# Performance work log

Measured on AMD Instinct MI355X. Metric: run time of the kernel, lower is better.

The kernel has to match this reference:

```python
import jax, jax.numpy as jnp
import numpy as np

ALPHA = 0.1
K = 10
N_NODES = 100000
N_EDGES = 3200000


def setup_inputs() -> dict:
    key = jax.random.key(0)
    ks = jax.random.split(key, 8)
    feat = jax.random.normal(ks[0], (N_NODES, 512), dtype=jnp.float32)
    W1 = jax.random.normal(ks[1], (512, 256), dtype=jnp.float32) * (1.0 / np.sqrt(512))
    b1 = jnp.zeros((256,), dtype=jnp.float32)
    W2 = jax.random.normal(ks[2], (256, 64), dtype=jnp.float32) * (1.0 / np.sqrt(256))
    b2 = jnp.zeros((64,), dtype=jnp.float32)
    edge_vals = jax.random.uniform(ks[3], (N_EDGES,), dtype=jnp.float32) / 32.0  # ~row-normalized
    edge_row = jax.random.randint(ks[4], (N_EDGES,), 0, N_NODES, dtype=jnp.int32)
    edge_col = jax.random.randint(ks[5], (N_EDGES,), 0, N_NODES, dtype=jnp.int32)
    return {"features": feat, "W1": W1, "b1": b1, "W2": W2, "b2": b2,
            "edge_vals": edge_vals, "edge_row": edge_row, "edge_col": edge_col}


def _spmm(edge_vals, edge_row, edge_col, x):
    # out[r] = sum_e vals[e] * x[col[e]]  for edges with row[e]==r
    msgs = edge_vals[:, None] * x[edge_col]  # [E, C]
    return jax.ops.segment_sum(msgs, edge_row, num_segments=N_NODES)


def reference(features, W1, b1, W2, b2, edge_vals, edge_row, edge_col):
    # MLP (dropout is identity in eval mode)
    x = jax.nn.relu(features @ W1 + b1)        # [N, nhid]
    x = x @ W2 + b2                             # [N, num_classes]
    h = x
    for _ in range(K):
        x = (1.0 - ALPHA) * _spmm(edge_vals, edge_row, edge_col, x) + ALPHA * h
    return jax.nn.log_softmax(x, axis=1)
```

## Files before the change

### kernel.cpp

```cpp
#include <hip/hip_runtime.h>
#include <hip/hip_bf16.h>
#include <math.h>

#define NNODES 100000
#define NFEAT 512
#define NHID 256
#define NCLS 64
#define ALPHA_C 0.1f
#define NBUCKET 512
#define NPB 512
#define RB2 196

typedef short s16x8 __attribute__((ext_vector_type(8)));
typedef float f32x4 __attribute__((ext_vector_type(4)));

__device__ inline unsigned short f2b(float f) {
    union { float f; unsigned u; } v; v.f = f;
    unsigned r = v.u + 0x7fff + ((v.u >> 16) & 1);
    return (unsigned short)(r >> 16);
}
__device__ inline float b2f(unsigned short b) {
    return __uint_as_float((unsigned)b << 16);
}
__device__ inline float blo(unsigned u) { return __uint_as_float(u << 16); }
__device__ inline float bhi(unsigned u) { return __uint_as_float(u & 0xffff0000u); }

__global__ __launch_bounds__(256) void cvtT_kernel(
    const float* __restrict__ src, unsigned short* __restrict__ dst, int R, int Clog2)
{
    int idx = blockIdx.x * 256 + threadIdx.x;
    int C = 1 << Clog2;
    if (idx < R * C) {
        int r = idx >> Clog2, c = idx & (C - 1);
        dst[(size_t)c * R + r] = f2b(src[idx]);
    }
}

#define HID_STRIDE 264

__global__ __launch_bounds__(256) void mlp_mfma_kernel(
    const float* __restrict__ feat, const unsigned short* __restrict__ W1T,
    const float* __restrict__ b1, const unsigned short* __restrict__ W2T,
    const float* __restrict__ b2, unsigned short* __restrict__ h, int N)
{
    __shared__ unsigned short hid_s[64 * HID_STRIDE];
    const int tid  = threadIdx.x;
    const int w    = tid >> 6;
    const int lane = tid & 63;
    const int lr   = lane & 15;
    const int lh   = lane >> 4;
    const int m0   = blockIdx.x * 64;

    f32x4 acc[4][4];
#pragma unroll
    for (int i = 0; i < 4; ++i)
#pragma unroll
        for (int j = 0; j < 4; ++j) acc[i][j] = (f32x4)0.f;

    const float* arow[4];
#pragma unroll
    for (int mi = 0; mi < 4; ++mi) {
        int r = m0 + mi * 16 + lr;
        if (r > N - 1) r = N - 1;
        arow[mi] = feat + (size_t)r * NFEAT;
    }
    const unsigned short* brow[4];
#pragma unroll
    for (int nj = 0; nj < 4; ++nj)
        brow[nj] = W1T + (size_t)(w * 64 + nj * 16 + lr) * NFEAT;

    for (int kb = 0; kb < NFEAT; kb += 32) {
        const int k0 = kb + lh * 8;
        s16x8 afr[4], bfr[4];
#pragma unroll
        for (int mi = 0; mi < 4; ++mi) {
            float4 f0 = *reinterpret_cast<const float4*>(arow[mi] + k0);
            float4 f1 = *reinterpret_cast<const float4*>(arow[mi] + k0 + 4);
            s16x8 a;
            a[0] = f2b(f0.x); a[1] = f2b(f0.y); a[2] = f2b(f0.z); a[3] = f2b(f0.w);
            a[4] = f2b(f1.x); a[5] = f2b(f1.y); a[6] = f2b(f1.z); a[7] = f2b(f1.w);
            afr[mi] = a;
        }
#pragma unroll
        for (int nj = 0; nj < 4; ++nj)
            bfr[nj] = *reinterpret_cast<const s16x8*>(brow[nj] + k0);
#pragma unroll
        for (int mi = 0; mi < 4; ++mi)
#pragma unroll
            for (int nj = 0; nj < 4; ++nj)
                acc[mi][nj] = __builtin_amdgcn_mfma_f32_16x16x32_bf16(
                    afr[mi], bfr[nj], acc[mi][nj], 0, 0, 0);
    }

#pragma unroll
    for (int nj = 0; nj < 4; ++nj) {
        int col = w * 64 + nj * 16 + lr;
        float bias = b1[col];
#pragma unroll
        for (int mi = 0; mi < 4; ++mi)
#pragma unroll
            for (int q = 0; q < 4; ++q) {
                int row = mi * 16 + lh * 4 + q;
                hid_s[row * HID_STRIDE + col] = f2b(fmaxf(acc[mi][nj][q] + bias, 0.f));
            }
    }
    __syncthreads();

    f32x4 acc2[4];
#pragma unroll
    for (int i = 0; i < 4; ++i) acc2[i] = (f32x4)0.f;
    const int cw = w * 16;
    const unsigned short* b2row = W2T + (size_t)(cw + lr) * NHID;
    for (int ks = 0; ks < NHID; ks += 32) {
        int k0 = ks + lh * 8;
        s16x8 bfr = *reinterpret_cast<const s16x8*>(b2row + k0);
#pragma unroll
        for (int mi = 0; mi < 4; ++mi) {
            s16x8 afr = *reinterpret_cast<const s16x8*>(
                &hid_s[(mi * 16 + lr) * HID_STRIDE + k0]);
            acc2[mi] = __builtin_amdgcn_mfma_f32_16x16x32_bf16(afr, bfr, acc2[mi], 0, 0, 0);
        }
    }
    int col = cw + lr;
    float bias2 = b2[col];
#pragma unroll
    for (int mi = 0; mi < 4; ++mi)
#pragma unroll
        for (int q = 0; q < 4; ++q) {
            int row = m0 + mi * 16 + lh * 4 + q;
            if (row < N) h[(size_t)row * NCLS + col] = f2b(acc2[mi][q] + bias2);
        }
}

__global__ __launch_bounds__(1024) void scanA_kernel(
    const int* __restrict__ cnt, int* __restrict__ excl, int* __restrict__ partials, int n)
{
    __shared__ int wsum[16];
    const int t = threadIdx.x, wid = t >> 6, lane = t & 63;
    const int i = blockIdx.x * 1024 + t;
    int c = (i < n) ? cnt[i] : 0;
    int x = c;
#pragma unroll
    for (int off = 1; off < 64; off <<= 1) {
        int y = __shfl_up(x, off);
        if (lane >= off) x += y;
    }
    if (lane == 63) wsum[wid] = x;
    __syncthreads();
    if (wid == 0 && lane < 16) {
        int wv = wsum[lane];
#pragma unroll
        for (int off = 1; off < 16; off <<= 1) {
            int y = __shfl_up(wv, off);
            if (lane >= off) wv += y;
        }
        wsum[lane] = wv;
    }
    __syncthreads();
    int woff = wid ? wsum[wid - 1] : 0;
    int incl = x + woff;
    if (i < n) excl[i] = incl - c;
    if (t == 1023) partials[blockIdx.x] = incl;
}

__global__ __launch_bounds__(256) void scanB_kernel(
    int* __restrict__ partials, int* __restrict__ total_out, int nb, int n)
{
    __shared__ int s[256];
    const int t = threadIdx.x;
    int v = (t < nb) ? partials[t] : 0;
    s[t] = v;
    __syncthreads();
    for (int off = 1; off < 256; off <<= 1) {
        int y = (t >= off) ? s[t - off] : 0;
        __syncthreads();
        s[t] += y;
        __syncthreads();
    }
    partials[t] = s[t] - v;
    if (t == 255) total_out[n] = s[255];
}

__global__ __launch_bounds__(1024) void scanC_kernel(
    int* __restrict__ arr, const int* __restrict__ partials, int n)
{
    const int i = blockIdx.x * 1024 + threadIdx.x;
    if (i < n) arr[i] += partials[blockIdx.x];
}

__global__ __launch_bounds__(256) void countP1_kernel(
    const int* __restrict__ erow, int* __restrict__ cnts, int E, int CE)
{
    __shared__ int c[NBUCKET];
    const int blk = blockIdx.x, t = threadIdx.x;
    for (int i = t; i < NBUCKET; i += 256) c[i] = 0;
    __syncthreads();
    const int e0 = blk * CE, e1 = min(e0 + CE, E);
    for (int e = e0 + t; e < e1; e += 256)
        atomicAdd(&c[erow[e] / RB2], 1);
    __syncthreads();
    for (int b = t; b < NBUCKET; b += 256)
        cnts[(size_t)b * NPB + blk] = c[b];
}

__global__ __launch_bounds__(256) void scatterA_kernel(
    const float* __restrict__ vals, const int* __restrict__ erow,
    const int* __restrict__ ecol, const int* __restrict__ S,
    unsigned long long* __restrict__ stage, int E, int CE)
{
    __shared__ int lcur[NBUCKET];
    const int blk = blockIdx.x, t = threadIdx.x;
    for (int b = t; b < NBUCKET; b += 256) lcur[b] = S[(size_t)b * NPB + blk];
    __syncthreads();
    const int e0 = blk * CE, e1 = min(e0 + CE, E);
    for (int e = e0 + t; e < e1; e += 256) {
        int r = erow[e];
        unsigned q = (unsigned)__float2int_rn(vals[e] * 1048576.f);
        if (q > 32767u) q = 32767u;
        unsigned lo = ((unsigned)ecol[e] << 15) | q;
        int pos = atomicAdd(&lcur[r / RB2], 1);
        stage[pos] = ((unsigned long long)(unsigned)r << 32) | lo;
    }
}

__global__ __launch_bounds__(256) void scatterB_kernel(
    const unsigned long long* __restrict__ stage, const int* __restrict__ S,
    unsigned* __restrict__ ep, int* __restrict__ row_ptr, int n, int E)
{
    __shared__ int hcnt[256];
    __shared__ int lcur[256];
    const int b = blockIdx.x, t = threadIdx.x;
    if (b == 0 && t == 0) row_ptr[n] = E;
    const int r0 = b * RB2;
    if (r0 >= n) return;
    const int nr = min(RB2, n - r0);
    const int s0 = S[(size_t)b * NPB];
    const int s1 = S[(size_t)(b + 1) * NPB];
    hcnt[t] = 0;
    __syncthreads();
    for (int i = s0 + t; i < s1; i += 256)
        atomicAdd(&hcnt[(int)(stage[i] >> 32) - r0], 1);
    __syncthreads();
    int v = hcnt[t];
    lcur[t] = v;
    __syncthreads();
    for (int off = 1; off < 256; off <<= 1) {
        int y = (t >= off) ? lcur[t - off] : 0;
        __syncthreads();
        lcur[t] += y;
        __syncthreads();
    }
    int excl = lcur[t] - v;
    if (t < nr) row_ptr[r0 + t] = s0 + excl;
    __syncthreads();
    lcur[t] = s0 + excl;
    __syncthreads();
    for (int i = s0 + t; i < s1; i += 256) {
        unsigned long long rec = stage[i];
        int p = atomicAdd(&lcur[(int)(rec >> 32) - r0], 1);
        ep[p] = (unsigned)rec;
    }
}

__global__ __launch_bounds__(256) void spmm_kernel(
    const unsigned short* __restrict__ x_in, const unsigned short* __restrict__ h,
    unsigned short* __restrict__ x_out, const int* __restrict__ row_ptr,
    const unsigned* __restrict__ ep, int n)
{
    const int wid = threadIdx.x >> 6, lane = threadIdx.x & 63;
    const int r = blockIdx.x * 4 + wid;
    if (r >= n) return;
    const int g  = lane >> 4;
    const int li = lane & 15;
    const int s = row_ptr[r], e_end = row_ptr[r + 1];

    float aA0 = 0.f, aA1 = 0.f, aA2 = 0.f, aA3 = 0.f;
    float aB0 = 0.f, aB1 = 0.f, aB2 = 0.f, aB3 = 0.f;
    float aC0 = 0.f, aC1 = 0.f, aC2 = 0.f, aC3 = 0.f;
    float aD0 = 0.f, aD1 = 0.f, aD2 = 0.f, aD3 = 0.f;
    int e0 = s;
    for (; e0 + 16 <= e_end; e0 += 16) {
        unsigned p1 = __builtin_nontemporal_load(ep + e0 + g);
        unsigned p2 = __builtin_nontemporal_load(ep + e0 + 4 + g);
        unsigned p3 = __builtin_nontemporal_load(ep + e0 + 8 + g);
        unsigned p4 = __builtin_nontemporal_load(ep + e0 + 12 + g);
        int   c1 = (int)(p1 >> 15);
        int   c2 = (int)(p2 >> 15);
        int   c3 = (int)(p3 >> 15);
        int   c4 = (int)(p4 >> 15);
        float v1 = (float)(p1 & 0x7fffu) * (1.f / 1048576.f);
        float v2 = (float)(p2 & 0x7fffu) * (1.f / 1048576.f);
        float v3 = (float)(p3 & 0x7fffu) * (1.f / 1048576.f);
        float v4 = (float)(p4 & 0x7fffu) * (1.f / 1048576.f);
        uint2 u1 = *reinterpret_cast<const uint2*>(x_in + ((size_t)c1 << 6) + (li << 2));
        uint2 u2 = *reinterpret_cast<const uint2*>(x_in + ((size_t)c2 << 6) + (li << 2));
        uint2 u3 = *reinterpret_cast<const uint2*>(x_in + ((size_t)c3 << 6) + (li << 2));
        uint2 u4 = *reinterpret_cast<const uint2*>(x_in + ((size_t)c4 << 6) + (li << 2));
        aA0 += v1 * blo(u1.x); aA1 += v1 * bhi(u1.x);
        aA2 += v1 * blo(u1.y); aA3 += v1 * bhi(u1.y);
        aB0 += v2 * blo(u2.x); aB1 += v2 * bhi(u2.x);
        aB2 += v2 * blo(u2.y); aB3 += v2 * bhi(u2.y);
        aC0 += v3 * blo(u3.x); aC1 += v3 * bhi(u3.x);
        aC2 += v3 * blo(u3.y); aC3 += v3 * bhi(u3.y);
        aD0 += v4 * blo(u4.x); aD1 += v4 * bhi(u4.x);
        aD2 += v4 * blo(u4.y); aD3 += v4 * bhi(u4.y);
    }
    for (; e0 < e_end; e0 += 4) {
        int e = e0 + g;
        if (e < e_end) {
            unsigned p = __builtin_nontemporal_load(ep + e);
            int   c = (int)(p >> 15);
            float v = (float)(p & 0x7fffu) * (1.f / 1048576.f);
            uint2 u = *reinterpret_cast<const uint2*>(x_in + ((size_t)c << 6) + (li << 2));
            aA0 += v * blo(u.x); aA1 += v * bhi(u.x);
            aA2 += v * blo(u.y); aA3 += v * bhi(u.y);
        }
    }
    float a0 = (aA0 + aB0) + (aC0 + aD0);
    float a1 = (aA1 + aB1) + (aC1 + aD1);
    float a2 = (aA2 + aB2) + (aC2 + aD2);
    float a3 = (aA3 + aB3) + (aC3 + aD3);
#pragma unroll
    for (int off = 16; off < 64; off <<= 1) {
        a0 += __shfl_xor(a0, off);
        a1 += __shfl_xor(a1, off);
        a2 += __shfl_xor(a2, off);
        a3 += __shfl_xor(a3, off);
    }
    if (g == 0) {
        size_t o = ((size_t)r << 6) + (li << 2);
        const unsigned* hp = reinterpret_cast<const unsigned*>(h + o);
        unsigned hx = __builtin_nontemporal_load(hp);
        unsigned hy = __builtin_nontemporal_load(hp + 1);
        float r0 = (1.f - ALPHA_C) * a0 + ALPHA_C * blo(hx);
        float r1 = (1.f - ALPHA_C) * a1 + ALPHA_C * bhi(hx);
        float r2 = (1.f - ALPHA_C) * a2 + ALPHA_C * blo(hy);
        float r3 = (1.f - ALPHA_C) * a3 + ALPHA_C * bhi(hy);
        uint2 ou;
        ou.x = ((unsigned)f2b(r1) << 16) | f2b(r0);
        ou.y = ((unsigned)f2b(r3) << 16) | f2b(r2);
        *reinterpret_cast<uint2*>(x_out + o) = ou;
    }
}

__global__ __launch_bounds__(256) void lsm_kernel(
    const unsigned short* __restrict__ x, float* __restrict__ out, int n)
{
    const int wid = threadIdx.x >> 6, lane = threadIdx.x & 63;
    const int r = blockIdx.x * 4 + wid;
    if (r >= n) return;
    float v = b2f(x[(size_t)r * NCLS + lane]);
    float m = v;
#pragma unroll
    for (int o = 32; o > 0; o >>= 1) m = fmaxf(m, __shfl_xor(m, o));
    float ex = expf(v - m);
    float s = ex;
#pragma unroll
    for (int o = 32; o > 0; o >>= 1) s += __shfl_xor(s, o);
    out[(size_t)r * NCLS + lane] = (v - m) - logf(s);
}

extern "C" void kernel_launch(void* const* d_in, const int* in_sizes, int n_in,
                              void* d_out, int out_size, void* d_ws, size_t ws_size,
                              hipStream_t stream)
{
    const float* feat = (const float*)d_in[0];
    const float* W1   = (const float*)d_in[1];
    const float* b1   = (const float*)d_in[2];
    const float* W2   = (const float*)d_in[3];
    const float* b2   = (const float*)d_in[4];
    const float* vals = (const float*)d_in[5];
    const int*   erow = (const int*)d_in[6];
    const int*   ecol = (const int*)d_in[7];
    const int N = in_sizes[0] / NFEAT;
    const int E = in_sizes[5];
    float* out = (float*)d_out;
    const int CE = (E + NPB - 1) / NPB;
    const int NC = NBUCKET * NPB;

    size_t off = 0;
    auto alloc = [&](size_t bytes) -> void* {
        void* p = (char*)d_ws + off;
        off += (bytes + 255) & ~(size_t)255;
        return p;
    };
    unsigned short*     h        = (unsigned short*)alloc((size_t)N * NCLS * 2);
    unsigned short*     xA       = (unsigned short*)alloc((size_t)N * NCLS * 2);
    unsigned short*     xB       = (unsigned short*)alloc((size_t)N * NCLS * 2);
    int*                row_ptr  = (int*)alloc((size_t)(N + 1) * 4);
    int*                cnts     = (int*)alloc((size_t)NC * 4);
    int*                S        = (int*)alloc((size_t)(NC + 1) * 4);
    int*                partials = (int*)alloc(256 * 4);
    unsigned*           ep       = (unsigned*)alloc((size_t)E * 4);
    unsigned long long* stage    = (unsigned long long*)alloc((size_t)E * 8);
    unsigned short*     W1T      = (unsigned short*)alloc((size_t)NHID * NFEAT * 2);
    unsigned short*     W2T      = (unsigned short*)alloc((size_t)NCLS * NHID * 2);
    (void)ws_size;

    cvtT_kernel<<<(NFEAT * NHID + 255) / 256, 256, 0, stream>>>(W1, W1T, NFEAT, 8);
    cvtT_kernel<<<(NHID * NCLS + 255) / 256, 256, 0, stream>>>(W2, W2T, NHID, 6);

    mlp_mfma_kernel<<<(N + 63) / 64, 256, 0, stream>>>(feat, W1T, b1, W2T, b2, h, N);

    countP1_kernel<<<NPB, 256, 0, stream>>>(erow, cnts, E, CE);
    scanA_kernel<<<NC / 1024, 1024, 0, stream>>>(cnts, S, partials, NC);
    scanB_kernel<<<1, 256, 0, stream>>>(partials, S, 256, NC);
    scanC_kernel<<<NC / 1024, 1024, 0, stream>>>(S, partials, NC);
    scatterA_kernel<<<NPB, 256, 0, stream>>>(vals, erow, ecol, S, stage, E, CE);
    scatterB_kernel<<<NBUCKET, 256, 0, stream>>>(stage, S, ep, row_ptr, N, E);

    const int gprop = (N + 3) / 4;
    const unsigned short* cur = h;
    for (int i = 0; i < 10; ++i) {
        unsigned short* dst = (i & 1) ? xB : xA;
        spmm_kernel<<<gprop, 256, 0, stream>>>(cur, h, dst, row_ptr, ep, N);
        cur = dst;
    }

    lsm_kernel<<<(N + 3) / 4, 256, 0, stream>>>(cur, out, N);
}
```

Baseline: 1.076 ms.

## Split propagation into four 16-column groups for cache-resident gathers

Stores the MLP output in a column-grouped layout of four slabs of 16 bf16 columns per node. Each slab is propagated through all ten SpMM iterations independently, so the gathered working set (about 3.2 MB per slab) can stay in L2 or the last-level cache instead of streaming 12.8 MB of random rows. The cost is four times as many launches and four times the edge-list reads, and each gather now moves only 4 bytes per lane. The log-softmax kernel is updated to read the grouped layout.

```diff
diff --git a/kernel.cpp b/kernel.cpp
--- a/kernel.cpp
+++ b/kernel.cpp
@@ -123,12 +123,13 @@
     }
     int col = cw + lr;
     float bias2 = b2[col];
+    const size_t cbase = (size_t)(col >> 4) * N * 16 + (col & 15);
 #pragma unroll
     for (int mi = 0; mi < 4; ++mi)
 #pragma unroll
         for (int q = 0; q < 4; ++q) {
             int row = m0 + mi * 16 + lh * 4 + q;
-            if (row < N) h[(size_t)row * NCLS + col] = f2b(acc2[mi][q] + bias2);
+            if (row < N) h[cbase + (size_t)row * 16] = f2b(acc2[mi][q] + bias2);
         }
 }
 
@@ -257,89 +258,60 @@
     __syncthreads();
     for (int i = s0 + t; i < s1; i += 256) {
         unsigned long long rec = stage[i];
-        int p = atomicAdd(&lcur[(int)(rec >> 32) - r0], 1);
+        int r = (int)(rec >> 32);
+        int p = atomicAdd(&lcur[r - r0], 1);
         ep[p] = (unsigned)rec;
     }
 }
 
 __global__ __launch_bounds__(256) void spmm_kernel(
-    const unsigned short* __restrict__ x_in, const unsigned short* __restrict__ h,
-    unsigned short* __restrict__ x_out, const int* __restrict__ row_ptr,
+    const unsigned short* __restrict__ xg, const unsigned short* __restrict__ hg,
+    unsigned short* __restrict__ og, const int* __restrict__ row_ptr,
     const unsigned* __restrict__ ep, int n)
 {
     const int wid = threadIdx.x >> 6, lane = threadIdx.x & 63;
     const int r = blockIdx.x * 4 + wid;
     if (r >= n) return;
-    const int g  = lane >> 4;
-    const int li = lane & 15;
+    const int sub = lane >> 3;
+    const int li  = lane & 7;
     const int s = row_ptr[r], e_end = row_ptr[r + 1];
 
-    float aA0 = 0.f, aA1 = 0.f, aA2 = 0.f, aA3 = 0.f;
-    float aB0 = 0.f, aB1 = 0.f, aB2 = 0.f, aB3 = 0.f;
-    float aC0 = 0.f, aC1 = 0.f, aC2 = 0.f, aC3 = 0.f;
-    float aD0 = 0.f, aD1 = 0.f, aD2 = 0.f, aD3 = 0.f;
+    float aA0 = 0.f, aA1 = 0.f, aB0 = 0.f, aB1 = 0.f;
     int e0 = s;
     for (; e0 + 16 <= e_end; e0 += 16) {
-        unsigned p1 = __builtin_nontemporal_load(ep + e0 + g);
-        unsigned p2 = __builtin_nontemporal_load(ep + e0 + 4 + g);
-        unsigned p3 = __builtin_nontemporal_load(ep + e0 + 8 + g);
-        unsigned p4 = __builtin_nontemporal_load(ep + e0 + 12 + g);
+        unsigned p1 = __builtin_nontemporal_load(ep + e0 + sub);
+        unsigned p2 = __builtin_nontemporal_load(ep + e0 + 8 + sub);
         int   c1 = (int)(p1 >> 15);
         int   c2 = (int)(p2 >> 15);
-        int   c3 = (int)(p3 >> 15);
-        int   c4 = (int)(p4 >> 15);
         float v1 = (float)(p1 & 0x7fffu) * (1.f / 1048576.f);
         float v2 = (float)(p2 & 0x7fffu) * (1.f / 1048576.f);
-        float v3 = (float)(p3 & 0x7fffu) * (1.f / 1048576.f);
-        float v4 = (float)(p4 & 0x7fffu) * (1.f / 1048576.f);
-        uint2 u1 = *reinterpret_cast<const uint2*>(x_in + ((size_t)c1 << 6) + (li << 2));
-        uint2 u2 = *reinterpret_cast<const uint2*>(x_in + ((size_t)c2 << 6) + (li << 2));
-        uint2 u3 = *reinterpret_cast<const uint2*>(x_in + ((size_t)c3 << 6) + (li << 2));
-        uint2 u4 = *reinterpret_cast<const uint2*>(x_in + ((size_t)c4 << 6) + (li << 2));
-        aA0 += v1 * blo(u1.x); aA1 += v1 * bhi(u1.x);
-        aA2 += v1 * blo(u1.y); aA3 += v1 * bhi(u1.y);
-        aB0 += v2 * blo(u2.x); aB1 += v2 * bhi(u2.x);
-        aB2 += v2 * blo(u2.y); aB3 += v2 * bhi(u2.y);
-        aC0 += v3 * blo(u3.x); aC1 += v3 * bhi(u3.x);
-        aC2 += v3 * blo(u3.y); aC3 += v3 * bhi(u3.y);
-        aD0 += v4 * blo(u4.x); aD1 += v4 * bhi(u4.x);
-        aD2 += v4 * blo(u4.y); aD3 += v4 * bhi(u4.y);
-    }
-    for (; e0 < e_end; e0 += 4) {
-        int e = e0 + g;
+        unsigned u1 = *reinterpret_cast<const unsigned*>(xg + ((size_t)c1 << 4) + (li << 1));
+        unsigned u2 = *reinterpret_cast<const unsigned*>(xg + ((size_t)c2 << 4) + (li << 1));
+        aA0 += v1 * blo(u1); aA1 += v1 * bhi(u1);
+        aB0 += v2 * blo(u2); aB1 += v2 * bhi(u2);
+    }
+    for (; e0 < e_end; e0 += 8) {
+        int e = e0 + sub;
         if (e < e_end) {
             unsigned p = __builtin_nontemporal_load(ep + e);
             int   c = (int)(p >> 15);
             float v = (float)(p & 0x7fffu) * (1.f / 1048576.f);
-            uint2 u = *reinterpret_cast<const uint2*>(x_in + ((size_t)c << 6) + (li << 2));
-            aA0 += v * blo(u.x); aA1 += v * bhi(u.x);
-            aA2 += v * blo(u.y); aA3 += v * bhi(u.y);
-        }
-    }
-    float a0 = (aA0 + aB0) + (aC0 + aD0);
-    float a1 = (aA1 + aB1) + (aC1 + aD1);
-    float a2 = (aA2 + aB2) + (aC2 + aD2);
-    float a3 = (aA3 + aB3) + (aC3 + aD3);
-#pragma unroll
-    for (int off = 16; off < 64; off <<= 1) {
+            unsigned u = *reinterpret_cast<const unsigned*>(xg + ((size_t)c << 4) + (li << 1));
+            aA0 += v * blo(u); aA1 += v * bhi(u);
+        }
+    }
+    float a0 = aA0 + aB0, a1 = aA1 + aB1;
+#pragma unroll
+    for (int off = 8; off < 64; off <<= 1) {
         a0 += __shfl_xor(a0, off);
         a1 += __shfl_xor(a1, off);
-        a2 += __shfl_xor(a2, off);
-        a3 += __shfl_xor(a3, off);
-    }
-    if (g == 0) {
-        size_t o = ((size_t)r << 6) + (li << 2);
-        const unsigned* hp = reinterpret_cast<const unsigned*>(h + o);
-        unsigned hx = __builtin_nontemporal_load(hp);
-        unsigned hy = __builtin_nontemporal_load(hp + 1);
-        float r0 = (1.f - ALPHA_C) * a0 + ALPHA_C * blo(hx);
-        float r1 = (1.f - ALPHA_C) * a1 + ALPHA_C * bhi(hx);
-        float r2 = (1.f - ALPHA_C) * a2 + ALPHA_C * blo(hy);
-        float r3 = (1.f - ALPHA_C) * a3 + ALPHA_C * bhi(hy);
-        uint2 ou;
-        ou.x = ((unsigned)f2b(r1) << 16) | f2b(r0);
-        ou.y = ((unsigned)f2b(r3) << 16) | f2b(r2);
-        *reinterpret_cast<uint2*>(x_out + o) = ou;
+    }
+    if (sub == 0) {
+        size_t o = ((size_t)r << 4) + (li << 1);
+        unsigned hu = *reinterpret_cast<const unsigned*>(hg + o);
+        float r0 = (1.f - ALPHA_C) * a0 + ALPHA_C * blo(hu);
+        float r1 = (1.f - ALPHA_C) * a1 + ALPHA_C * bhi(hu);
+        *reinterpret_cast<unsigned*>(og + o) = ((unsigned)f2b(r1) << 16) | f2b(r0);
     }
 }
 
@@ -349,7 +321,7 @@
     const int wid = threadIdx.x >> 6, lane = threadIdx.x & 63;
     const int r = blockIdx.x * 4 + wid;
     if (r >= n) return;
-    float v = b2f(x[(size_t)r * NCLS + lane]);
+    float v = b2f(x[(size_t)(lane >> 4) * n * 16 + (size_t)r * 16 + (lane & 15)]);
     float m = v;
 #pragma unroll
     for (int o = 32; o > 0; o >>= 1) m = fmaxf(m, __shfl_xor(m, o));
@@ -410,12 +382,15 @@
     scatterB_kernel<<<NBUCKET, 256, 0, stream>>>(stage, S, ep, row_ptr, N, E);
 
     const int gprop = (N + 3) / 4;
-    const unsigned short* cur = h;
-    for (int i = 0; i < 10; ++i) {
-        unsigned short* dst = (i & 1) ? xB : xA;
-        spmm_kernel<<<gprop, 256, 0, stream>>>(cur, h, dst, row_ptr, ep, N);
-        cur = dst;
-    }
-
-    lsm_kernel<<<(N + 3) / 4, 256, 0, stream>>>(cur, out, N);
-}
+    for (int g = 0; g < 4; ++g) {
+        const size_t goff = (size_t)g * N * 16;
+        const unsigned short* cur = h + goff;
+        for (int i = 0; i < 10; ++i) {
+            unsigned short* dst = ((i & 1) ? xB : xA) + goff;
+            spmm_kernel<<<gprop, 256, 0, stream>>>(cur, h + goff, dst, row_ptr, ep, N);
+            cur = dst;
+        }
+    }
+
+    lsm_kernel<<<gprop, 256, 0, stream>>>(xB, out, N);
+}
```

Result: slower. 2.229 ms (+107.2%).
